# Kernel tuning notes

Measured on AMD Instinct MI355X. Metric: run time of the kernel, lower is better.

## Reference

```python
import jax, jax.numpy as jnp
import numpy as np

B, C, H, W = 8, 256, 96, 96
NQ, NCLS = 100, 12
OBJ_CH = NCLS - 2 + 1  # 11
EPS = 1e-6


def conv2d(x, w, b, pad):
    out = jax.lax.conv_general_dilated(x, w, (1, 1), [(pad, pad), (pad, pad)],
                                       dimension_numbers=('NCHW', 'OIHW', 'NCHW'))
    return out + b[None, :, None, None]


def conv1d(x, w, b):
    out = jax.lax.conv_general_dilated(x, w, (1,), [(0, 0)],
                                       dimension_numbers=('NCH', 'OIH', 'NCH'))
    return out + b[None, :, None]


def adaptive_avg_pool_1d(x, out_size):
    # x: [..., L]; torch AdaptiveAvgPool semantics: bin i = mean(x[floor(i*L/o):ceil((i+1)*L/o)])
    L = x.shape[-1]
    i = np.arange(out_size)
    starts = (i * L) // out_size
    ends = -((-(i + 1) * L) // out_size)
    csum = jnp.concatenate([jnp.zeros(x.shape[:-1] + (1,), x.dtype), jnp.cumsum(x, -1)], -1)
    sizes = jnp.asarray((ends - starts).astype(np.float32))
    return (csum[..., ends] - csum[..., starts]) / sizes


def local_max(p):
    # 8-neighbor local maximum with zero padding, thresholded at EPS
    pd = jnp.pad(p, ((0, 0), (0, 0), (1, 1), (1, 1)))
    m = ((p >= pd[:, :, :-2, 1:-1]) & (p >= pd[:, :, 2:, 1:-1]) &
         (p >= pd[:, :, 1:-1, :-2]) & (p >= pd[:, :, 1:-1, 2:]) &
         (p >= pd[:, :, :-2, :-2]) & (p >= pd[:, :, :-2, 2:]) &
         (p >= pd[:, :, 2:, :-2]) & (p >= pd[:, :, 2:, 2:]) & (p >= EPS))
    return m.astype(p.dtype)


def mask_and_nms(probs):
    # one-hot mask from argmax over foreground channels, then add local-max map
    oh = jax.nn.one_hot(jnp.argmax(probs[:, :-1], axis=1), probs.shape[1], axis=1, dtype=probs.dtype)
    p = probs * oh
    return p + local_max(p)


def head(x, w1, b1, w2, b2):
    return conv2d(jax.nn.relu(conv2d(x, w1, b1, 1)), w2, b2, 0)


def setup_inputs() -> dict:
    key = jax.random.key(0)
    ks = jax.random.split(key, 20)
    rn = lambda k, s: jax.random.normal(k, s, jnp.float32) * 0.02
    z = lambda n: jnp.zeros((n,), jnp.float32)
    return {
        'x': jax.random.normal(ks[0], (B, C, H, W), jnp.float32),
        'y': jax.random.normal(ks[1], (B, C, H, W), jnp.float32),
        'pos_embeddings': jax.random.normal(ks[2], (1, C, H, W), jnp.float32),
        'lw1': rn(ks[3], (C, C, 3, 3)), 'lb1': z(C),
        'lw2': rn(ks[4], (2, C, 1, 1)), 'lb2': z(2),
        'rw1': rn(ks[5], (C, C, 3, 3)), 'rb1': z(C),
        'rw2': rn(ks[6], (2, C, 1, 1)), 'rb2': z(2),
        'ow1': rn(ks[7], (C, C, 3, 3)), 'ob1': z(C),
        'ow2': rn(ks[8], (OBJ_CH, C, 1, 1)), 'ob2': z(OBJ_CH),
        'cw1': rn(ks[9], (64, C, 3, 3)), 'cb1': z(64),
        'cw2': rn(ks[10], (32, 64, 3, 3)), 'cb2': z(32),
        'cm_lw': rn(ks[11], (778 * 2, 778 * 32)), 'cm_lb': z(778 * 2),
        'c1d_w': rn(ks[12], (C, 2, 3)), 'c1d_b': z(C),
        'q_lw': rn(ks[13], (NQ * C, C)), 'q_lb': z(NQ * C),
    }


def reference(x, y, pos_embeddings, lw1, lb1, lw2, lb2, rw1, rb1, rw2, rb2,
              ow1, ob1, ow2, ob2, cw1, cb1, cw2, cb2, cm_lw, cm_lb,
              c1d_w, c1d_b, q_lw, q_lb):
    b = x.shape[0]
    left_logits = head(x, lw1, lb1, lw2, lb2)
    right_logits = head(x, rw1, rb1, rw2, rb2)
    obj_logits = head(x, ow1, ob1, ow2, ob2)

    left_p = mask_and_nms(jax.nn.softmax(left_logits, axis=1))
    right_p = mask_and_nms(jax.nn.softmax(right_logits, axis=1))
    obj_p = mask_and_nms(jax.nn.softmax(obj_logits, axis=1))

    hw = H * W
    idx_l = jax.lax.top_k(left_p[:, 0].reshape(b, hw), 40)[1]
    idx_r = jax.lax.top_k(right_p[:, 0].reshape(b, hw), 40)[1]
    idx_o = jax.lax.top_k(obj_p[:, :-1].reshape(b, OBJ_CH - 1, hw).max(axis=1), 20)[1]
    idx = jnp.concatenate([idx_l, idx_r, idx_o], axis=1)  # [B, 100]

    xf = x.reshape(b, C, hw)
    topk_proposals = jnp.take_along_axis(xf, jnp.broadcast_to(idx[:, None, :], (b, C, NQ)), axis=2)
    pf = jnp.broadcast_to(pos_embeddings, (b, C, H, W)).reshape(b, C, hw)
    topk_pos = jnp.take_along_axis(pf, jnp.broadcast_to(idx[:, None, :], (b, C, NQ)), axis=2)

    # contact map estimation branch
    h = jax.nn.relu(conv2d(y, cw1, cb1, 1))
    h = jax.nn.relu(conv2d(h, cw2, cb2, 1))  # [B,32,H,W]
    h = jnp.mean(h, axis=3)                  # adaptive pool width -> 1
    h = adaptive_avg_pool_1d(h, 778)         # [B,32,778]
    cm = h.reshape(b, -1) @ cm_lw.T + cm_lb  # [B,1556]
    contact_map = cm.reshape(b, 2, 778, 1)

    # ContactMapConvolution
    cc = conv1d(contact_map.reshape(b, 2, 778), c1d_w, c1d_b)  # [B,C,776]
    cc = jnp.mean(cc, axis=2)                                  # [B,C]
    feat = (cc @ q_lw.T + q_lb).reshape(b, C, NQ)              # [B,C,100]

    topk_proposals = topk_proposals + feat
    return (topk_proposals, topk_pos, left_logits, right_logits, obj_logits, contact_map)
```

## Files before the change

kernel.cpp:

```cpp
#include <hip/hip_runtime.h>
#include <float.h>
#include <math.h>

#define B_ 8
#define C_ 256
#define H_ 96
#define W_ 96
#define HW_ 9216
#define NQ_ 100
#define EPS_ 1e-6f
#define PADW_ 98
#define PADIMG_ 9604
#define PALLOC_ 76880

typedef unsigned short ushort_t;
typedef __attribute__((ext_vector_type(8))) short bf16x8;
typedef __attribute__((ext_vector_type(16))) float f32x16;

typedef __attribute__((address_space(3))) unsigned int as3_u32;
typedef __attribute__((address_space(1))) unsigned int as1_u32;

__device__ __forceinline__ void gl16(const void* g, void* l) {
    __builtin_amdgcn_global_load_lds(
        (const as1_u32*)(unsigned long long)g,
        (as3_u32*)(unsigned int)(unsigned long long)l, 16, 0, 0);
}

__device__ __forceinline__ ushort_t bf16_of(float v) {
    unsigned u = __float_as_uint(v);
    u += 0x7fffu + ((u >> 16) & 1u);
    return (ushort_t)(u >> 16);
}
__device__ __forceinline__ float f_of_bf16(ushort_t h) {
    return __uint_as_float((unsigned)h << 16);
}

__global__ __launch_bounds__(256)
void zero_border_kernel(ushort_t* __restrict__ bh, ushort_t* __restrict__ bl, int Cch)
{
    int per = 388 * Cch / 8;
    int id = blockIdx.x * 256 + threadIdx.x;
    if (id >= 8 * per) return;
    int b = id / per, i = id - b * per;
    int pi = (i * 8) / Cch, c8 = (i * 8) % Cch;
    int yy, xx;
    if (pi < 98)      { yy = 0;            xx = pi; }
    else if (pi < 196){ yy = 97;           xx = pi - 98; }
    else if (pi < 292){ yy = pi - 195;     xx = 0; }
    else              { yy = pi - 291;     xx = 97; }
    size_t base = ((size_t)b * PADIMG_ + yy * PADW_ + xx) * Cch + c8;
    *(bf16x8*)&bh[base] = (bf16x8)(short)0;
    *(bf16x8*)&bl[base] = (bf16x8)(short)0;
}

__global__ __launch_bounds__(256)
void tsplit_kernel(const float* __restrict__ in, ushort_t* __restrict__ oh,
                   ushort_t* __restrict__ ol, int Cch)
{
    __shared__ float T[32][33];
    const int tx = threadIdx.x & 31, ty = threadIdx.x >> 5;
    const int p0 = blockIdx.x * 32, ci0 = blockIdx.y * 32, b = blockIdx.z;
#pragma unroll
    for (int i = 0; i < 4; ++i)
        T[ty + 8*i][tx] = in[((size_t)b*Cch + ci0 + ty + 8*i)*HW_ + p0 + tx];
    __syncthreads();
    const int y = p0 / 96, x0 = p0 - y * 96;
    const size_t Pp = (size_t)b*PADIMG_ + (size_t)(y + 1)*PADW_ + x0 + 1;
#pragma unroll
    for (int i = 0; i < 4; ++i) {
        float v = T[tx][ty + 8*i];
        ushort_t hi = bf16_of(v);
        float lo = v - f_of_bf16(hi);
        size_t o = (Pp + ty + 8*i)*Cch + ci0 + tx;
        oh[o] = hi;
        ol[o] = bf16_of(lo);
    }
}

__global__ __launch_bounds__(256)
void repack_kernel(const float* __restrict__ w, ushort_t* __restrict__ wh,
                   ushort_t* __restrict__ wl, int Cout, int Cin)
{
    int id = blockIdx.x*256 + threadIdx.x;
    int tot = 9*Cout*Cin;
    if (id >= tot) return;
    int tap = id / (Cout*Cin);
    int r   = id - tap*(Cout*Cin);
    int g   = r / (Cout*16);
    int r2  = r - g*(Cout*16);
    int oc  = r2 >> 4, cr = r2 & 15;
    int ci  = g*16 + cr;
    float v = w[((size_t)oc*Cin + ci)*9 + tap];
    ushort_t hi = bf16_of(v);
    wh[id] = hi;
    wl[id] = bf16_of(v - f_of_bf16(hi));
}

__global__ __launch_bounds__(256)
void pack_heads3_kernel(const float* lb1, const float* rb1, const float* ob1,
                        const float* lw2, const float* rw2, const float* ow2,
                        const float* lb2, const float* rb2, const float* ob2,
                        float* __restrict__ bias1all, float* __restrict__ w2all,
                        float* __restrict__ b2all)
{
    int i = blockIdx.x * 256 + threadIdx.x;
    if (i < 768) bias1all[i] = (i < 256) ? lb1[i] : (i < 512) ? rb1[i-256] : ob1[i-512];
    if (i < 33) {
        int h = i / 11, k = i - h*11;
        b2all[i] = (h == 0) ? (k < 2 ? lb2[k] : 0.f)
                 : (h == 1) ? (k < 2 ? rb2[k] : 0.f)
                 : ob2[k];
    }
    if (i < 3*11*256) {
        int h = i / 2816, r = i - h*2816;
        int k = r / 256, oc = r - k*256;
        float v = 0.f;
        if (h == 0)      { if (k < 2) v = lw2[k*256 + oc]; }
        else if (h == 1) { if (k < 2) v = rw2[k*256 + oc]; }
        else             v = ow2[k*256 + oc];
        w2all[i] = v;
    }
}

template<int WM, int WN, int MFR, int NFR, int CIN, int MODE>
__global__ __launch_bounds__(WM*WN*64, (WM*WN + 3) / 4)
void conv_gemm_kernel(const ushort_t* __restrict__ Agh, const ushort_t* __restrict__ Agl,
                      const ushort_t* __restrict__ Wgh, const ushort_t* __restrict__ Wgl,
                      const float* __restrict__ bias1,
                      ushort_t* __restrict__ Oth, ushort_t* __restrict__ Otl,
                      float* __restrict__ outf)
{
    constexpr int NW    = WM*WN;
    constexpr int NT    = NW*64;
    constexpr int BM    = WM*MFR*32;
    constexpr int COUT  = WN*NFR*32;
    constexpr int NG    = CIN/16;
    constexpr int APAD  = 512;
    constexpr int ASZ   = 2*APAD*16;
    constexpr int AROUNDS = 32;
    static_assert(BM == 288, "BM must be 288");

    __shared__ __align__(16) ushort_t ALds[2*ASZ];

    const int tid  = threadIdx.x;
    const int lane = tid & 63;
    const int wid  = __builtin_amdgcn_readfirstlane(tid >> 6);
    const int wm   = wid / WN, wn = wid % WN;
    const int l31  = lane & 31, hh2 = lane >> 5;
    const int wnb  = wn * NFR * 32;

    const int cpx = gridDim.x >> 3;
    const int bid = (blockIdx.x & 7)*cpx + (blockIdx.x >> 3);
    const int bidx = bid >> 5;
    const int br   = bid & 31;
    const size_t S = (size_t)bidx*PADIMG_ + (size_t)(3*br)*PADW_;

    auto stageA = [&](int g, int sel) {
        ushort_t* dst = ALds + sel*ASZ;
#pragma unroll 1
        for (int c = wid; c < AROUNDS; c += NW) {
            int id = c*64 + lane;
            int split = id >> 10;
            int r2 = id & 1023;
            int row = r2 >> 1, slot = r2 & 1;
            int ch = slot ^ ((row >> 2) & 1);
            const ushort_t* src = (split ? Agl : Agh) + (S + row)*CIN + g*16 + ch*8;
            gl16(src, dst + (size_t)c*512);
        }
    };

    f32x16 acc[MFR][NFR];
#pragma unroll
    for (int i = 0; i < MFR; ++i)
#pragma unroll
        for (int j = 0; j < NFR; ++j)
#pragma unroll
            for (int r = 0; r < 16; ++r) acc[i][j][r] = 0.f;

    bf16x8 bh0[NFR], bl0[NFR], bh1[NFR], bl1[NFR], bh2[NFR], bl2[NFR];

#define LOADB(G, T, BH, BL)                                                    \
    {                                                                          \
        _Pragma("unroll")                                                      \
        for (int nf = 0; nf < NFR; ++nf) {                                     \
            size_t o = ((size_t)((T)*NG + (G))*COUT + (wnb + nf*32 + l31))*16  \
                       + hh2*8;                                                \
            BH[nf] = *(const bf16x8*)&Wgh[o];                                  \
            BL[nf] = *(const bf16x8*)&Wgl[o];                                  \
        }                                                                      \
    }

    stageA(0, 0);
    LOADB(0, 0, bh0, bl0);
    LOADB(0, 1, bh1, bl1);
    __builtin_amdgcn_sched_barrier(0);
    asm volatile("s_waitcnt vmcnt(%0)" :: "n"(4*NFR) : "memory");
    __builtin_amdgcn_s_barrier();
    __builtin_amdgcn_sched_barrier(0);

#define TAPBODY(T, BHC, BLC, BHN, BLN)                                         \
    {                                                                          \
        if ((T) <= 6)            LOADB(g,     (T)+2, BHN, BLN)                 \
        else if (g + 1 < NG)     LOADB(g+1,   (T)-7, BHN, BLN)                 \
        const int tapoff = ((T)/3)*PADW_ + ((T) % 3);                          \
        _Pragma("unroll")                                                      \
        for (int mf = 0; mf < MFR; ++mf) {                                     \
            int row = wm*PADW_ + tapoff + mf*32 + l31;                         \
            int o = abase + row*16 + ((hh2 ^ ((row >> 2) & 1)) << 3);          \
            bf16x8 ah = *(const bf16x8*)&ALds[o];                              \
            bf16x8 al = *(const bf16x8*)&ALds[o + APAD*16];                    \
            _Pragma("unroll")                                                  \
            for (int nf = 0; nf < NFR; ++nf) {                                 \
                acc[mf][nf] = __builtin_amdgcn_mfma_f32_32x32x16_bf16(         \
                    ah, BHC[nf], acc[mf][nf], 0, 0, 0);                        \
                acc[mf][nf] = __builtin_amdgcn_mfma_f32_32x32x16_bf16(         \
                    al, BHC[nf], acc[mf][nf], 0, 0, 0);                        \
                acc[mf][nf] = __builtin_amdgcn_mfma_f32_32x32x16_bf16(         \
                    ah, BLC[nf], acc[mf][nf], 0, 0, 0);                        \
            }                                                                  \
        }                                                                      \
    }

#pragma unroll 1
    for (int g = 0; g < NG; ++g) {
        if (g + 1 < NG) stageA(g + 1, (g + 1) & 1);
        const int abase = (g & 1) * ASZ;
        TAPBODY(0, bh0, bl0, bh2, bl2);
        TAPBODY(1, bh1, bl1, bh0, bl0);
        TAPBODY(2, bh2, bl2, bh1, bl1);
        TAPBODY(3, bh0, bl0, bh2, bl2);
        TAPBODY(4, bh1, bl1, bh0, bl0);
        TAPBODY(5, bh2, bl2, bh1, bl1);
        TAPBODY(6, bh0, bl0, bh2, bl2);
        TAPBODY(7, bh1, bl1, bh0, bl0);
        TAPBODY(8, bh2, bl2, bh1, bl1);
        __builtin_amdgcn_sched_barrier(0);
        asm volatile("s_waitcnt lgkmcnt(0)" ::: "memory");
        asm volatile("s_waitcnt vmcnt(%0)" :: "n"(4*NFR) : "memory");
        __builtin_amdgcn_s_barrier();
        __builtin_amdgcn_sched_barrier(0);
    }
#undef TAPBODY
#undef LOADB
    __syncthreads();

    float biasv[NFR];
#pragma unroll
    for (int nf = 0; nf < NFR; ++nf) biasv[nf] = bias1[wnb + nf*32 + l31];

    if constexpr (MODE == 1) {
#pragma unroll
        for (int mf = 0; mf < MFR; ++mf)
#pragma unroll
            for (int nf = 0; nf < NFR; ++nf)
#pragma unroll
                for (int r = 0; r < 16; ++r) {
                    float rr = fmaxf(acc[mf][nf][r] + biasv[nf], 0.f);
                    ushort_t hi = bf16_of(rr);
                    float lo = rr - f_of_bf16(hi);
                    int crow = (r & 3) + 8*(r >> 2) + 4*hh2;
                    int xx = mf*32 + crow;
                    size_t Pp = (size_t)bidx*PADIMG_
                              + (size_t)(3*br + wm + 1)*PADW_ + xx + 1;
                    size_t o = Pp*COUT + wnb + nf*32 + l31;
                    Oth[o] = hi;
                    Otl[o] = bf16_of(lo);
                }
    } else {
        float (*T)[BM + 1] = (float(*)[BM + 1])ALds;
#pragma unroll
        for (int mf = 0; mf < MFR; ++mf)
#pragma unroll
            for (int r = 0; r < 16; ++r) {
                float rr = fmaxf(acc[mf][0][r] + biasv[0], 0.f);
                int crow = (r & 3) + 8*(r >> 2) + 4*hh2;
                T[l31][wm*96 + mf*32 + crow] = rr;
            }
        __syncthreads();
        for (int i = tid; i < COUT*BM; i += NT) {
            int c = i / BM, m = i - c*BM;
            outf[((size_t)bidx*COUT + c)*HW_ + br*288 + m] = T[c][m];
        }
    }
}

template<int KK, int NH>
__global__ __launch_bounds__(256, 3)
void conv_sbt_kernel(const ushort_t* __restrict__ Agh, const ushort_t* __restrict__ Agl,
                     const ushort_t* __restrict__ w0h, const ushort_t* __restrict__ w0l,
                     const ushort_t* __restrict__ w1h, const ushort_t* __restrict__ w1l,
                     const float* __restrict__ bias1base, const float* __restrict__ w2base,
                     const float* __restrict__ b2base, float* __restrict__ dstbase)
{
    constexpr int NG = 16, APAD = 304, ASZ = 2*APAD*16, AGR = 19, MFR = 3, NFR = 2;
    __shared__ __align__(16) ushort_t ALds[ASZ];

    const int tid  = threadIdx.x;
    const int lane = tid & 63;
    const int wid  = __builtin_amdgcn_readfirstlane(tid >> 6);
    const int l31  = lane & 31, hh2 = lane >> 5;
    const int wnb  = wid * 64;

    const int h    = (NH == 1) ? 0 : (blockIdx.x / 768);
    const int subx = blockIdx.x - h*768;
    const int sub  = (subx & 7)*96 + (subx >> 3);
    const int bidx = sub / 96, prow = sub - bidx*96;
    const int pimg0 = prow * 96;
    const size_t S = (size_t)bidx*PADIMG_ + (size_t)prow*PADW_;

    const ushort_t* Wh = (h == 0) ? w0h : w1h;
    const ushort_t* Wl = (h == 0) ? w0l : w1l;
    const float* bias1 = bias1base + h*256;
    const float* w2    = w2base + (size_t)h*2816;
    const float* b2    = b2base + h*11;
    float* dst = dstbase + (size_t)h*147456;

    auto stageA = [&](int g) {
#pragma unroll 1
        for (int c = wid; c < AGR; c += 4) {
            int id = c*64 + lane;
            int split = id / (2*APAD);
            int r2 = id % (2*APAD);
            int row = r2 >> 1, slot = r2 & 1;
            int ch = slot ^ ((row >> 2) & 1);
            const ushort_t* src = (split ? Agl : Agh) + (S + row)*C_ + g*16 + ch*8;
            gl16(src, ALds + (size_t)c*512);
        }
    };

    f32x16 acc[MFR][NFR];
#pragma unroll
    for (int i = 0; i < MFR; ++i)
#pragma unroll
        for (int j = 0; j < NFR; ++j)
#pragma unroll
            for (int r = 0; r < 16; ++r) acc[i][j][r] = 0.f;

    bf16x8 bhX[NFR], blX[NFR], bhY[NFR], blY[NFR];

#define LOADB(G, T, BH, BL)                                                    \
    {                                                                          \
        _Pragma("unroll")                                                      \
        for (int nf = 0; nf < NFR; ++nf) {                                     \
            size_t o = ((size_t)((T)*NG + (G))*256 + (wnb + nf*32 + l31))*16   \
                       + hh2*8;                                                \
            BH[nf] = *(const bf16x8*)&Wh[o];                                   \
            BL[nf] = *(const bf16x8*)&Wl[o];                                   \
        }                                                                      \
    }

#define TAPBODY(G, T, BHC, BLC, BHN, BLN)                                      \
    {                                                                          \
        if ((T) < 8)             LOADB((G), (T)+1, BHN, BLN)                   \
        else if ((G) + 1 < NG)   LOADB((G)+1, 0, BHN, BLN)                     \
        const int tapoff = ((T)/3)*PADW_ + ((T) % 3);                          \
        _Pragma("unroll")                                                      \
        for (int mf = 0; mf < MFR; ++mf) {                                     \
            int row = tapoff + mf*32 + l31;                                    \
            int o = row*16 + ((hh2 ^ ((row >> 2) & 1)) << 3);                  \
            bf16x8 ah = *(const bf16x8*)&ALds[o];                              \
            bf16x8 al = *(const bf16x8*)&ALds[o + APAD*16];                    \
            _Pragma("unroll")                                                  \
            for (int nf = 0; nf < NFR; ++nf) {                                 \
                acc[mf][nf] = __builtin_amdgcn_mfma_f32_32x32x16_bf16(         \
                    ah, BHC[nf], acc[mf][nf], 0, 0, 0);                        \
                acc[mf][nf] = __builtin_amdgcn_mfma_f32_32x32x16_bf16(         \
                    al, BHC[nf], acc[mf][nf], 0, 0, 0);                        \
                acc[mf][nf] = __builtin_amdgcn_mfma_f32_32x32x16_bf16(         \
                    ah, BLC[nf], acc[mf][nf], 0, 0, 0);                        \
            }                                                                  \
        }                                                                      \
    }

#define GROUPBODY(G, S0h, S0l, S1h, S1l)                                       \
    {                                                                          \
        TAPBODY((G), 0, S0h, S0l, S1h, S1l);                                   \
        TAPBODY((G), 1, S1h, S1l, S0h, S0l);                                   \
        TAPBODY((G), 2, S0h, S0l, S1h, S1l);                                   \
        TAPBODY((G), 3, S1h, S1l, S0h, S0l);                                   \
        TAPBODY((G), 4, S0h, S0l, S1h, S1l);                                   \
        TAPBODY((G), 5, S1h, S1l, S0h, S0l);                                   \
        TAPBODY((G), 6, S0h, S0l, S1h, S1l);                                   \
        TAPBODY((G), 7, S1h, S1l, S0h, S0l);                                   \
        TAPBODY((G), 8, S0h, S0l, S1h, S1l);                                   \
    }

#define STAGEWAIT(G)                                                           \
    __builtin_amdgcn_sched_barrier(0);                                         \
    asm volatile("s_waitcnt lgkmcnt(0)" ::: "memory");                         \
    __builtin_amdgcn_sched_barrier(0);                                         \
    __builtin_amdgcn_s_barrier();             \
    stageA(G);                                                                 \
    __builtin_amdgcn_sched_barrier(0);                                         \
    asm volatile("s_waitcnt vmcnt(0)" ::: "memory");                           \
    __builtin_amdgcn_s_barrier();                                              \
    __builtin_amdgcn_sched_barrier(0);

    LOADB(0, 0, bhX, blX);

#pragma unroll 1
    for (int g = 0; g < NG; g += 2) {
        STAGEWAIT(g)
        GROUPBODY(g,     bhX, blX, bhY, blY);
        STAGEWAIT(g + 1)
        GROUPBODY(g + 1, bhY, blY, bhX, blX);
    }
#undef STAGEWAIT
#undef GROUPBODY
#undef TAPBODY
#undef LOADB
    __syncthreads();

    float biasv[NFR];
#pragma unroll
    for (int nf = 0; nf < NFR; ++nf) biasv[nf] = bias1[wnb + nf*32 + l31];
    float w2v[NFR][KK];
#pragma unroll
    for (int nf = 0; nf < NFR; ++nf)
#pragma unroll
        for (int k = 0; k < KK; ++k) w2v[nf][k] = w2[k*256 + wnb + nf*32 + l31];

    float* Lacc = (float*)ALds;
#pragma unroll
    for (int mf = 0; mf < MFR; ++mf) {
#pragma unroll
        for (int r = 0; r < 16; ++r) {
            float v[KK];
#pragma unroll
            for (int k = 0; k < KK; ++k) v[k] = 0.f;
#pragma unroll
            for (int nf = 0; nf < NFR; ++nf) {
                float rr = fmaxf(acc[mf][nf][r] + biasv[nf], 0.f);
#pragma unroll
                for (int k = 0; k < KK; ++k) v[k] += rr * w2v[nf][k];
            }
#pragma unroll
            for (int k = 0; k < KK; ++k) {
                v[k] += __shfl_xor(v[k], 1);
                v[k] += __shfl_xor(v[k], 2);
                v[k] += __shfl_xor(v[k], 4);
                v[k] += __shfl_xor(v[k], 8);
                v[k] += __shfl_xor(v[k], 16);
            }
            if (l31 == 0) {
                int crow = (r & 3) + 8*(r >> 2) + 4*hh2;
                int row96 = mf*32 + crow;
#pragma unroll
                for (int k = 0; k < KK; ++k)
                    Lacc[((size_t)wid*96 + row96)*KK + k] = v[k];
            }
        }
    }
    __syncthreads();
    for (int i = tid; i < 96*KK; i += 256) {
        int row96 = i / KK, k = i - row96*KK;
        float s = b2[k];
#pragma unroll
        for (int w = 0; w < 4; ++w) s += Lacc[((size_t)w*96 + row96)*KK + k];
        dst[((size_t)bidx*KK + k)*HW_ + pimg0 + row96] = s;
    }
}

__global__ __launch_bounds__(256)
void prob2b_kernel(const float* __restrict__ l2, const float* __restrict__ l3,
                   float* __restrict__ pL, float* __restrict__ pR)
{
    const float* logits = blockIdx.y ? l3 : l2;
    float* p0 = blockIdx.y ? pR : pL;
    int i = blockIdx.x * 256 + threadIdx.x;
    if (i >= B_ * HW_) return;
    int b = i / HW_, pix = i - b * HW_;
    float l0 = logits[(size_t)b * 2 * HW_ + pix];
    float l1 = logits[(size_t)b * 2 * HW_ + HW_ + pix];
    float m = fmaxf(l0, l1);
    float e0 = expf(l0 - m), e1 = expf(l1 - m);
    p0[i] = e0 / (e0 + e1);
}

__global__ __launch_bounds__(256)
void score2b_kernel(const float* __restrict__ pL, const float* __restrict__ pR,
                    float* __restrict__ sL, float* __restrict__ sR)
{
    const float* p = blockIdx.y ? pR : pL;
    float* sc = blockIdx.y ? sR : sL;
    int i = blockIdx.x * 256 + threadIdx.x;
    if (i >= B_ * HW_) return;
    int pix = i % HW_;
    int yy = pix / W_, xx = pix - (pix / W_) * W_;
    float c = p[i];
    bool ok = (c >= EPS_);
    const float* pb = p + (i - pix);
#pragma unroll
    for (int dy = -1; dy <= 1; ++dy)
#pragma unroll
        for (int dx = -1; dx <= 1; ++dx) {
            if (dy == 0 && dx == 0) continue;
            int ny = yy + dy, nx = xx + dx;
            float v = 0.f;
            if (ny >= 0 && ny < H_ && nx >= 0 && nx < W_) v = pb[ny * W_ + nx];
            ok = ok && (c >= v);
        }
    sc[i] = c + (ok ? 1.f : 0.f);
}

__global__ __launch_bounds__(256)
void probobj_kernel(const float* __restrict__ logits, float* __restrict__ pval,
                    int* __restrict__ cstar)
{
    int i = blockIdx.x * 256 + threadIdx.x;
    if (i >= B_ * HW_) return;
    int b = i / HW_, pix = i - b * HW_;
    const float* lb = logits + (size_t)b * 11 * HW_ + pix;
    float l[11];
#pragma unroll
    for (int c2 = 0; c2 < 11; ++c2) l[c2] = lb[(size_t)c2 * HW_];
    float m = l[0];
#pragma unroll
    for (int c2 = 1; c2 < 11; ++c2) m = fmaxf(m, l[c2]);
    float sum = 0.f;
#pragma unroll
    for (int c2 = 0; c2 < 11; ++c2) sum += expf(l[c2] - m);
    int a = 0; float bestl = l[0];
#pragma unroll
    for (int c2 = 1; c2 < 10; ++c2)
        if (l[c2] > bestl) { bestl = l[c2]; a = c2; }
    pval[i] = expf(bestl - m) / sum;
    cstar[i] = a;
}

__global__ __launch_bounds__(256)
void score11_kernel(const float* __restrict__ p, const int* __restrict__ cs,
                    float* __restrict__ sc)
{
    int i = blockIdx.x * 256 + threadIdx.x;
    if (i >= B_ * HW_) return;
    int pix = i % HW_;
    int yy = pix / W_, xx = pix - (pix / W_) * W_;
    float c = p[i];
    int cc = cs[i];
    bool ok = (c >= EPS_);
    int base = i - pix;
#pragma unroll
    for (int dy = -1; dy <= 1; ++dy)
#pragma unroll
        for (int dx = -1; dx <= 1; ++dx) {
            if (dy == 0 && dx == 0) continue;
            int ny = yy + dy, nx = xx + dx;
            float v = 0.f;
            if (ny >= 0 && ny < H_ && nx >= 0 && nx < W_) {
                int n = base + ny * W_ + nx;
                v = (cs[n] == cc) ? p[n] : 0.f;
            }
            ok = ok && (c >= v);
        }
    sc[i] = c + (ok ? 1.f : 0.f);
}

__global__ __launch_bounds__(256)
void topk_kernel(const float* __restrict__ scL, const float* __restrict__ scR,
                 const float* __restrict__ scO, int* __restrict__ idx)
{
    __shared__ float sv[HW_];
    __shared__ float rv[256];
    __shared__ int   ri[256];
    const int h = blockIdx.x, b = blockIdx.y;
    const float* src = (h == 0) ? scL : (h == 1) ? scR : scO;
    const int k = (h == 2) ? 20 : 40;
    const int off = b * NQ_ + ((h == 0) ? 0 : (h == 1) ? 40 : 80);

    for (int t = threadIdx.x; t < HW_; t += 256) sv[t] = src[(size_t)b * HW_ + t];
    __syncthreads();

    for (int kk = 0; kk < k; ++kk) {
        float bestv = -FLT_MAX; int besti = HW_;
        for (int t = threadIdx.x; t < HW_; t += 256) {
            float v = sv[t];
            if (v > bestv) { bestv = v; besti = t; }
        }
        rv[threadIdx.x] = bestv; ri[threadIdx.x] = besti;
        __syncthreads();
        for (int s = 128; s > 0; s >>= 1) {
            if (threadIdx.x < s) {
                float v2 = rv[threadIdx.x + s]; int i2 = ri[threadIdx.x + s];
                if (v2 > rv[threadIdx.x] ||
                    (v2 == rv[threadIdx.x] && i2 < ri[threadIdx.x])) {
                    rv[threadIdx.x] = v2; ri[threadIdx.x] = i2;
                }
            }
            __syncthreads();
        }
        if (threadIdx.x == 0) { idx[off + kk] = ri[0]; sv[ri[0]] = -FLT_MAX; }
        __syncthreads();
    }
}

__global__ __launch_bounds__(128)
void pool_kernel(const float* __restrict__ h2, float* __restrict__ pooled)
{
    int bc = blockIdx.x;
    __shared__ float row[96];
    for (int hh = threadIdx.x; hh < 96; hh += 128) {
        const float* p = h2 + (size_t)bc * HW_ + hh * W_;
        float s = 0.f;
        for (int ww = 0; ww < 96; ++ww) s += p[ww];
        row[hh] = s * (1.f / 96.f);
    }
    __syncthreads();
    for (int i = threadIdx.x; i < 778; i += 128) {
        int s0 = (i * 96) / 778;
        int e0 = ((i + 1) * 96 + 777) / 778;
        float s = 0.f;
        for (int t = s0; t < e0; ++t) s += row[t];
        pooled[(size_t)bc * 778 + i] = s / (float)(e0 - s0);
    }
}

__global__ __launch_bounds__(256)
void cm_kernel(const float* __restrict__ pooled, const float* __restrict__ cm_lw,
               const float* __restrict__ cm_lb, float* __restrict__ out5)
{
    const int j = blockIdx.x;
    const float* wr = cm_lw + (size_t)j * 24896;
    float acc[8];
#pragma unroll
    for (int b = 0; b < 8; ++b) acc[b] = 0.f;
    for (int t = threadIdx.x; t < 24896; t += 256) {
        float w = wr[t];
#pragma unroll
        for (int b = 0; b < 8; ++b) acc[b] += w * pooled[(size_t)b * 24896 + t];
    }
    __shared__ float red[8][256];
#pragma unroll
    for (int b = 0; b < 8; ++b) red[b][threadIdx.x] = acc[b];
    __syncthreads();
    for (int s = 128; s > 0; s >>= 1) {
        if (threadIdx.x < s) {
#pragma unroll
            for (int b = 0; b < 8; ++b) red[b][threadIdx.x] += red[b][threadIdx.x + s];
        }
        __syncthreads();
    }
    if (threadIdx.x < 8)
        out5[(size_t)threadIdx.x * 1556 + j] = red[threadIdx.x][0] + cm_lb[j];
}

__global__ __launch_bounds__(256)
void c1d_kernel(const float* __restrict__ cmap, const float* __restrict__ w,
                const float* __restrict__ bias, float* __restrict__ ccmean)
{
    int b = blockIdx.x;
    __shared__ float r[2][778];
    __shared__ float T[2][3];
    for (int t = threadIdx.x; t < 1556; t += 256)
        r[t / 778][t % 778] = cmap[(size_t)b * 1556 + t];
    __syncthreads();
    if (threadIdx.x < 2) {
        int ic = threadIdx.x;
        float s = 0.f;
        for (int i2 = 0; i2 < 778; ++i2) s += r[ic][i2];
        T[ic][0] = s - r[ic][776] - r[ic][777];
        T[ic][1] = s - r[ic][0]   - r[ic][777];
        T[ic][2] = s - r[ic][0]   - r[ic][1];
    }
    __syncthreads();
    int oc = threadIdx.x;
    float a = 0.f;
#pragma unroll
    for (int ic = 0; ic < 2; ++ic)
#pragma unroll
        for (int k = 0; k < 3; ++k)
            a += w[oc * 6 + ic * 3 + k] * T[ic][k];
    ccmean[b * 256 + oc] = a / 776.f + bias[oc];
}

__global__ __launch_bounds__(256)
void feat_kernel(const float* __restrict__ ccmean, const float* __restrict__ q_lw,
                 const float* __restrict__ q_lb, float* __restrict__ feat)
{
    __shared__ float cc[8][256];
    for (int t = threadIdx.x; t < 2048; t += 256) cc[t >> 8][t & 255] = ccmean[t];
    __syncthreads();
    int j = blockIdx.x * 256 + threadIdx.x;
    const float* wr = q_lw + (size_t)j * 256;
    float acc[8];
#pragma unroll
    for (int b = 0; b < 8; ++b) acc[b] = 0.f;
    for (int c = 0; c < 256; ++c) {
        float wv = wr[c];
#pragma unroll
        for (int b = 0; b < 8; ++b) acc[b] += wv * cc[b][c];
    }
    float qb = q_lb[j];
#pragma unroll
    for (int b = 0; b < 8; ++b) feat[(size_t)b * 25600 + j] = acc[b] + qb;
}

__global__ __launch_bounds__(256)
void gather_kernel(const float* __restrict__ x, const float* __restrict__ pos,
                   const float* __restrict__ feat, const int* __restrict__ idx,
                   float* __restrict__ out0, float* __restrict__ out1)
{
    int t = blockIdx.x * 256 + threadIdx.x;
    if (t >= B_ * C_ * NQ_) return;
    int q = t % NQ_;
    int c2 = (t / NQ_) % C_;
    int b = t / (C_ * NQ_);
    int p = idx[b * NQ_ + q];
    out0[t] = x[((size_t)b * C_ + c2) * HW_ + p] + feat[(size_t)b * 25600 + c2 * NQ_ + q];
    out1[t] = pos[(size_t)c2 * HW_ + p];
}

extern "C" void kernel_launch(void* const* d_in, const int* in_sizes, int n_in,
                              void* d_out, int out_size, void* d_ws, size_t ws_size,
                              hipStream_t stream) {
    const float* x    = (const float*)d_in[0];
    const float* y    = (const float*)d_in[1];
    const float* pos  = (const float*)d_in[2];
    const float* lw1  = (const float*)d_in[3];  const float* lb1 = (const float*)d_in[4];
    const float* lw2  = (const float*)d_in[5];  const float* lb2 = (const float*)d_in[6];
    const float* rw1  = (const float*)d_in[7];  const float* rb1 = (const float*)d_in[8];
    const float* rw2  = (const float*)d_in[9];  const float* rb2 = (const float*)d_in[10];
    const float* ow1  = (const float*)d_in[11]; const float* ob1 = (const float*)d_in[12];
    const float* ow2  = (const float*)d_in[13]; const float* ob2 = (const float*)d_in[14];
    const float* cw1  = (const float*)d_in[15]; const float* cb1 = (const float*)d_in[16];
    const float* cw2  = (const float*)d_in[17]; const float* cb2 = (const float*)d_in[18];
    const float* cmlw = (const float*)d_in[19]; const float* cmlb = (const float*)d_in[20];
    const float* c1dw = (const float*)d_in[21]; const float* c1db = (const float*)d_in[22];
    const float* qlw  = (const float*)d_in[23]; const float* qlb  = (const float*)d_in[24];

    float* out  = (float*)d_out;
    float* out0 = out;
    float* out1 = out + 204800;
    float* out2 = out + 409600;
    float* out3 = out + 557056;
    float* out4 = out + 704512;
    float* out5 = out + 1515520;

    float* ws = (float*)d_ws;
    ushort_t* Rh   = (ushort_t*)(ws);
    ushort_t* Rl   = (ushort_t*)(ws + 9840640);
    ushort_t* h1h  = (ushort_t*)(ws + 19681280);
    ushort_t* h1l  = (ushort_t*)(ws + 22141440);
    float*    h2   = ws + 24601600;
    ushort_t* wLh  = (ushort_t*)(ws + 26960896);
    ushort_t* wLl  = (ushort_t*)(ws + 27255808);
    ushort_t* wRh  = (ushort_t*)(ws + 27550720);
    ushort_t* wRl  = (ushort_t*)(ws + 27845632);
    ushort_t* wOh  = (ushort_t*)(ws + 28140544);
    ushort_t* wOl  = (ushort_t*)(ws + 28435456);
    ushort_t* wc1h = (ushort_t*)(ws + 28730368);
    ushort_t* wc1l = (ushort_t*)(ws + 28804096);
    ushort_t* wc2h = (ushort_t*)(ws + 28877824);
    ushort_t* wc2l = (ushort_t*)(ws + 28887040);
    float* pooled  = ws + 28896256;
    float* ccmean  = ws + 29095424;
    float* feat    = ws + 29097472;
    float* pmapL   = ws + 29302272;
    int*   csmap   = (int*)(ws + 29376000);
    float* scL     = ws + 29449728;
    float* scR     = ws + 29523456;
    float* scO     = ws + 29597184;
    int*   idxb    = (int*)(ws + 29670912);
    float* bias1all= ws + 29671712;
    float* w2all   = ws + 29672480;
    float* b2all   = ws + 29680928;
    float* pmapR   = ws + 29680976;
    float* pmapO   = ws + 29754704;
    (void)in_sizes; (void)n_in; (void)out_size; (void)ws_size; (void)pos;

    zero_border_kernel<<<388, 256, 0, stream>>>(Rh, Rl, 256);
    zero_border_kernel<<<97,  256, 0, stream>>>(h1h, h1l, 64);
    repack_kernel<<<(9*256*256+255)/256, 256, 0, stream>>>(lw1, wLh, wLl, 256, 256);
    repack_kernel<<<(9*256*256+255)/256, 256, 0, stream>>>(rw1, wRh, wRl, 256, 256);
    repack_kernel<<<(9*256*256+255)/256, 256, 0, stream>>>(ow1, wOh, wOl, 256, 256);
    repack_kernel<<<(9*64*256+255)/256,  256, 0, stream>>>(cw1, wc1h, wc1l, 64, 256);
    repack_kernel<<<(9*32*64+255)/256,   256, 0, stream>>>(cw2, wc2h, wc2l, 32, 64);
    pack_heads3_kernel<<<33, 256, 0, stream>>>(lb1, rb1, ob1, lw2, rw2, ow2,
                                               lb2, rb2, ob2, bias1all, w2all, b2all);

    tsplit_kernel<<<dim3(288, 8, 8), 256, 0, stream>>>(y, Rh, Rl, 256);
    conv_gemm_kernel<3,2,3,1,256,1><<<256, 384, 0, stream>>>(
        Rh, Rl, wc1h, wc1l, cb1, h1h, h1l, nullptr);
    conv_gemm_kernel<3,1,3,1,64,2><<<256, 192, 0, stream>>>(
        h1h, h1l, wc2h, wc2l, cb2, nullptr, nullptr, h2);
    pool_kernel<<<256, 128, 0, stream>>>(h2, pooled);
    cm_kernel<<<1556, 256, 0, stream>>>(pooled, cmlw, cmlb, out5);
    c1d_kernel<<<8, 256, 0, stream>>>(out5, c1dw, c1db, ccmean);
    feat_kernel<<<100, 256, 0, stream>>>(ccmean, qlw, qlb, feat);

    tsplit_kernel<<<dim3(288, 8, 8), 256, 0, stream>>>(x, Rh, Rl, 256);
    conv_sbt_kernel<2,2><<<1536, 256, 0, stream>>>(
        Rh, Rl, wLh, wLl, wRh, wRl, bias1all, w2all, b2all, out2);
    conv_sbt_kernel<11,1><<<768, 256, 0, stream>>>(
        Rh, Rl, wOh, wOl, wOh, wOl, bias1all + 512, w2all + 2*2816,
        b2all + 22, out4);

    prob2b_kernel<<<dim3(288, 2), 256, 0, stream>>>(out2, out3, pmapL, pmapR);
    score2b_kernel<<<dim3(288, 2), 256, 0, stream>>>(pmapL, pmapR, scL, scR);
    probobj_kernel<<<288, 256, 0, stream>>>(out4, pmapO, csmap);
    score11_kernel<<<288, 256, 0, stream>>>(pmapO, csmap, scO);

    topk_kernel<<<dim3(3, 8), 256, 0, stream>>>(scL, scR, scO, idxb);
    gather_kernel<<<800, 256, 0, stream>>>(x, pos, feat, idxb, out0, out1);
}
```

Before: 1.147 ms.

## Double-buffer LDS activation tiles in fused conv head kernel

Doubles the LDS buffer for the activation tile so the global-to-LDS load of the next channel group is issued before computing the current group. Each group now ends with a single wait and barrier, instead of the earlier barrier, stage, full-drain sequence. The wait uses a vmcnt threshold so the weight prefetch loads may remain outstanding. The aim is to hide activation load latency behind MFMA work. The cost is twice the LDS per block, which could lower occupancy, and the wait counts must track the in-flight loads exactly.

Result: no change. 1.146 ms (-0.1%).

```diff
diff --git a/kernel.cpp b/kernel.cpp
--- a/kernel.cpp
+++ b/kernel.cpp
@@ -293,7 +293,7 @@
                      const float* __restrict__ b2base, float* __restrict__ dstbase)
 {
     constexpr int NG = 16, APAD = 304, ASZ = 2*APAD*16, AGR = 19, MFR = 3, NFR = 2;
-    __shared__ __align__(16) ushort_t ALds[ASZ];
+    __shared__ __align__(16) ushort_t ALds[2*ASZ];
 
     const int tid  = threadIdx.x;
     const int lane = tid & 63;
@@ -315,7 +315,8 @@
     const float* b2    = b2base + h*11;
     float* dst = dstbase + (size_t)h*147456;
 
-    auto stageA = [&](int g) {
+    auto stageA = [&](int g, int sel) {
+        ushort_t* dstl = ALds + sel*ASZ;
 #pragma unroll 1
         for (int c = wid; c < AGR; c += 4) {
             int id = c*64 + lane;
@@ -324,7 +325,7 @@
             int row = r2 >> 1, slot = r2 & 1;
             int ch = slot ^ ((row >> 2) & 1);
             const ushort_t* src = (split ? Agl : Agh) + (S + row)*C_ + g*16 + ch*8;
-            gl16(src, ALds + (size_t)c*512);
+            gl16(src, dstl + (size_t)c*512);
         }
     };
 
@@ -349,7 +350,7 @@
         }                                                                      \
     }
 
-#define TAPBODY(G, T, BHC, BLC, BHN, BLN)                                      \
+#define TAPBODY(G, T, ABASE, BHC, BLC, BHN, BLN)                               \
     {                                                                          \
         if ((T) < 8)             LOADB((G), (T)+1, BHN, BLN)                   \
         else if ((G) + 1 < NG)   LOADB((G)+1, 0, BHN, BLN)                     \
@@ -357,7 +358,7 @@
         _Pragma("unroll")                                                      \
         for (int mf = 0; mf < MFR; ++mf) {                                     \
             int row = tapoff + mf*32 + l31;                                    \
-            int o = row*16 + ((hh2 ^ ((row >> 2) & 1)) << 3);                  \
+            int o = (ABASE) + row*16 + ((hh2 ^ ((row >> 2) & 1)) << 3);        \
             bf16x8 ah = *(const bf16x8*)&ALds[o];                              \
             bf16x8 al = *(const bf16x8*)&ALds[o + APAD*16];                    \
             _Pragma("unroll")                                                  \
@@ -372,40 +373,43 @@
         }                                                                      \
     }
 
-#define GROUPBODY(G, S0h, S0l, S1h, S1l)                                       \
+#define GROUPBODY(G, ABASE, S0h, S0l, S1h, S1l)                                \
     {                                                                          \
-        TAPBODY((G), 0, S0h, S0l, S1h, S1l);                                   \
-        TAPBODY((G), 1, S1h, S1l, S0h, S0l);                                   \
-        TAPBODY((G), 2, S0h, S0l, S1h, S1l);                                   \
-        TAPBODY((G), 3, S1h, S1l, S0h, S0l);                                   \
-        TAPBODY((G), 4, S0h, S0l, S1h, S1l);                                   \
-        TAPBODY((G), 5, S1h, S1l, S0h, S0l);                                   \
-        TAPBODY((G), 6, S0h, S0l, S1h, S1l);                                   \
-        TAPBODY((G), 7, S1h, S1l, S0h, S0l);                                   \
-        TAPBODY((G), 8, S0h, S0l, S1h, S1l);                                   \
-    }
-
-#define STAGEWAIT(G)                                                           \
+        TAPBODY((G), 0, (ABASE), S0h, S0l, S1h, S1l);                          \
+        TAPBODY((G), 1, (ABASE), S1h, S1l, S0h, S0l);                          \
+        TAPBODY((G), 2, (ABASE), S0h, S0l, S1h, S1l);                          \
+        TAPBODY((G), 3, (ABASE), S1h, S1l, S0h, S0l);                          \
+        TAPBODY((G), 4, (ABASE), S0h, S0l, S1h, S1l);                          \
+        TAPBODY((G), 5, (ABASE), S1h, S1l, S0h, S0l);                          \
+        TAPBODY((G), 6, (ABASE), S0h, S0l, S1h, S1l);                          \
+        TAPBODY((G), 7, (ABASE), S1h, S1l, S0h, S0l);                          \
+        TAPBODY((G), 8, (ABASE), S0h, S0l, S1h, S1l);                          \
+    }
+
+#define GROUPEND                                                               \
     __builtin_amdgcn_sched_barrier(0);                                         \
     asm volatile("s_waitcnt lgkmcnt(0)" ::: "memory");                         \
-    __builtin_amdgcn_sched_barrier(0);                                         \
-    __builtin_amdgcn_s_barrier();             \
-    stageA(G);                                                                 \
-    __builtin_amdgcn_sched_barrier(0);                                         \
-    asm volatile("s_waitcnt vmcnt(0)" ::: "memory");                           \
+    asm volatile("s_waitcnt vmcnt(%0)" :: "n"(2*NFR) : "memory");              \
     __builtin_amdgcn_s_barrier();                                              \
     __builtin_amdgcn_sched_barrier(0);
 
+    stageA(0, 0);
     LOADB(0, 0, bhX, blX);
+    __builtin_amdgcn_sched_barrier(0);
+    asm volatile("s_waitcnt vmcnt(%0)" :: "n"(2*NFR) : "memory");
+    __builtin_amdgcn_s_barrier();
+    __builtin_amdgcn_sched_barrier(0);
 
 #pragma unroll 1
     for (int g = 0; g < NG; g += 2) {
-        STAGEWAIT(g)
-        GROUPBODY(g,     bhX, blX, bhY, blY);
-        STAGEWAIT(g + 1)
-        GROUPBODY(g + 1, bhY, blY, bhX, blX);
-    }
-#undef STAGEWAIT
+        if (g + 1 < NG) stageA(g + 1, 1);
+        GROUPBODY(g, 0, bhX, blX, bhY, blY);
+        GROUPEND
+        if (g + 2 < NG) stageA(g + 2, 0);
+        GROUPBODY(g + 1, ASZ, bhY, blY, bhX, blX);
+        GROUPEND
+    }
+#undef GROUPEND
 #undef GROUPBODY
 #undef TAPBODY
 #undef LOADB
```
